# Kernel optimization log

Measured on AMD Instinct MI355X. Metric: run time of the kernel, lower is better.

Reference implementation:

```python
import jax, jax.numpy as jnp
from jax import lax
import numpy as np

VOCAB, EMBED, HID, MAXLEN, BATCH = 50000, 512, 1024, 100, 512
FORGET_BIAS = 2.0


def setup_inputs() -> dict:
    key = jax.random.key(0)
    ks = jax.random.split(key, 12)
    s = 0.02
    input_queries = jax.random.randint(ks[0], (BATCH, MAXLEN), 0, VOCAB, dtype=jnp.int32)
    input_replies = jax.random.randint(ks[1], (BATCH, MAXLEN), 0, VOCAB, dtype=jnp.int32)
    query_lengths = jnp.maximum(jax.random.randint(ks[2], (BATCH,), 0, MAXLEN, dtype=jnp.int32), 1)
    reply_lengths = jnp.maximum(jax.random.randint(ks[3], (BATCH,), 0, MAXLEN, dtype=jnp.int32), 1)
    embeddings = jax.random.normal(ks[4], (VOCAB, EMBED), dtype=jnp.float32) * s
    # shared peephole LSTM weights (reuse=True in the original): kernel over [x; h], gate order i, j, f, o
    W = jax.random.normal(ks[5], (EMBED + HID, 4 * HID), dtype=jnp.float32) * s
    b = jnp.zeros((4 * HID,), dtype=jnp.float32)
    p_i = jax.random.normal(ks[6], (HID,), dtype=jnp.float32) * s
    p_f = jax.random.normal(ks[7], (HID,), dtype=jnp.float32) * s
    p_o = jax.random.normal(ks[8], (HID,), dtype=jnp.float32) * s
    M = jax.random.normal(ks[9], (HID, HID), dtype=jnp.float32) * s
    return {
        "embeddings": embeddings, "W": W, "b": b,
        "p_i": p_i, "p_f": p_f, "p_o": p_o, "M": M,
        "input_queries": input_queries, "input_replies": input_replies,
        "query_lengths": query_lengths, "reply_lengths": reply_lengths,
    }


def _lstm_encode(x_emb, lengths, W, b, p_i, p_f, p_o):
    """Peephole LSTM (TF LSTMCell, use_peepholes=True). Returns final h at sequence_length."""
    B, L, _ = x_emb.shape
    H = p_i.shape[0]

    def step(carry, xt):
        c, h = carry
        x_t, t = xt                      # x_t: [B, E]
        z = jnp.concatenate([x_t, h], axis=-1) @ W + b   # [B, 4H]
        zi, zj, zf, zo = jnp.split(z, 4, axis=-1)
        i = jax.nn.sigmoid(zi + p_i * c)
        f = jax.nn.sigmoid(zf + FORGET_BIAS + p_f * c)
        c_new = f * c + i * jnp.tanh(zj)
        o = jax.nn.sigmoid(zo + p_o * c_new)
        h_new = o * jnp.tanh(c_new)
        valid = (t < lengths)[:, None]   # hold state past sequence_length
        return (jnp.where(valid, c_new, c), jnp.where(valid, h_new, h)), None

    init = (jnp.zeros((B, H), x_emb.dtype), jnp.zeros((B, H), x_emb.dtype))
    xs = (jnp.swapaxes(x_emb, 0, 1), jnp.arange(L, dtype=jnp.int32))
    (_, h), _ = lax.scan(step, init, xs)
    return h


def reference(embeddings, W, b, p_i, p_f, p_o, M,
              input_queries, input_replies, query_lengths, reply_lengths):
    q_emb = embeddings[input_queries]    # [B, L, E]
    r_emb = embeddings[input_replies]
    q_enc = _lstm_encode(q_emb, query_lengths, W, b, p_i, p_f, p_o)   # [B, H]
    r_enc = _lstm_encode(r_emb, reply_lengths, W, b, p_i, p_f, p_o)
    q_t = q_enc @ M                                                    # bilinear transform
    distances = q_t @ r_enc.T                                          # [B, B]
    # positives = diagonal, negatives = all off-diagonal (in-batch negatives)
    labels = jnp.eye(distances.shape[0], dtype=distances.dtype)
    # sigmoid cross entropy: softplus(x) - label * x, mean over all B*B logits
    loss = jnp.mean(jax.nn.softplus(distances) - labels * distances)
    return distances, loss
```

## Files before the change

kernel.cpp:

```cpp
#include <hip/hip_runtime.h>
#include <stdint.h>

typedef unsigned short u16;
typedef __bf16 bf16x8 __attribute__((ext_vector_type(8)));
typedef float f32x4 __attribute__((ext_vector_type(4)));

#define AS1 __attribute__((address_space(1)))
#define AS3 __attribute__((address_space(3)))

__device__ __forceinline__ void ld_lds16(const void* gp, void* lp) {
  __builtin_amdgcn_global_load_lds((AS1 void*)(void*)gp, (AS3 void*)lp, 16, 0, 0);
}

__device__ __forceinline__ u16 f2bf(float f) {
  uint32_t u = __float_as_uint(f);
  u += 0x7FFFu + ((u >> 16) & 1u);
  return (u16)(u >> 16);
}

__device__ __forceinline__ float fsig(float x) { return 1.0f / (1.0f + __expf(-x)); }
__device__ __forceinline__ float ftanhf(float x) {
  float e = __expf(-2.0f * fabsf(x));
  float t = (1.0f - e) / (1.0f + e);
  return copysignf(t, x);
}

#define LSEQ 100
#define EMB 512
#define HID 1024
#define KDIM 1536

__global__ __launch_bounds__(256, 2) void k_step(
    const u16* __restrict__ emb, const u16* __restrict__ W2T,
    const float* __restrict__ b2, const float* __restrict__ p_i,
    const float* __restrict__ p_f, const float* __restrict__ p_o,
    const int* __restrict__ tokQ, const int* __restrict__ tokR,
    const int* __restrict__ lenQ, const int* __restrict__ lenR,
    const u16* __restrict__ h_cur, u16* __restrict__ h_nxt,
    float* __restrict__ c_st, int t)
{
  __shared__ u16 sb[3 * 12288];
  const int tid = threadIdx.x;
  const int lane = tid & 63, wid = tid >> 6;
  const int wm = wid >> 1, wn = wid & 1;
  const int lane_lo = lane & 15, lane_hi = lane >> 4;
  const int g = blockIdx.x;
  const int bx = (g & 7) * 4 + ((g >> 3) & 3);
  const int by = g >> 5;

  f32x4 acc[2][4];
  const f32x4 zz = {0.f, 0.f, 0.f, 0.f};
#pragma unroll
  for (int a = 0; a < 2; ++a)
#pragma unroll
    for (int bb = 0; bb < 4; ++bb) acc[a][bb] = zz;

  int tokv[2], rowe[2], rowi[2], ldsoA[2], srcoA[2];
#pragma unroll
  for (int j = 0; j < 2; ++j) {
    const int ch = j * 256 + tid;
    const int r = ch >> 3;
    const int srcoff = ((ch & 7) ^ (r & 7)) * 8;
    const int m = by * 64 + r, e = m >> 9, i = m & 511;
    tokv[j] = (e ? tokR : tokQ)[i * LSEQ + t];
    rowe[j] = e; rowi[j] = i;
    srcoA[j] = srcoff;
    ldsoA[j] = ch * 8;
  }

  const int colbase = bx * 128 + wn * 64;
  const int h = ((colbase >> 6) << 4) + lane_lo;
  float b2v[4];
#pragma unroll
  for (int gg = 0; gg < 4; ++gg) b2v[gg] = b2[colbase + gg * 16 + lane_lo];
  const float pi = p_i[h], pf = p_f[h], po = p_o[h];
  int lenv[2][4];
  float cold[2][4];
  u16 hprev[2][4];
#pragma unroll
  for (int mi = 0; mi < 2; ++mi)
#pragma unroll
    for (int r = 0; r < 4; ++r) {
      const int m = by * 64 + wm * 32 + mi * 16 + lane_hi * 4 + r;
      const int e = m >> 9, i = m & 511;
      lenv[mi][r] = e ? lenR[i] : lenQ[i];
      const size_t ci = (size_t)(e * 512 + i) * HID + h;
      cold[mi][r] = c_st[ci];
      hprev[mi][r] = h_cur[ci];
    }
  __builtin_amdgcn_sched_barrier(0);

  const u16* pAx[2];
  const u16* pAh[2];
  const u16* pB[4];
  int ldsoB[4];
#pragma unroll
  for (int j = 0; j < 2; ++j) {
    pAx[j] = emb + (size_t)tokv[j] * EMB + srcoA[j];
    pAh[j] = h_cur + (size_t)(rowe[j] * 512 + rowi[j]) * HID - 512 + srcoA[j];
  }
#pragma unroll
  for (int j = 0; j < 4; ++j) {
    const int ch = j * 256 + tid;
    const int r = ch >> 3;
    const int srcoff = ((ch & 7) ^ (r & 7)) * 8;
    pB[j] = W2T + (size_t)(bx * 128 + r) * KDIM + srcoff;
    ldsoB[j] = ch * 8;
  }

  auto stage = [&](int kt, int buf) {
    const int kb = kt * 64;
    u16* lA = sb + buf * 12288;
    u16* lB = lA + 4096;
    const bool isx = kb < EMB;
#pragma unroll
    for (int j = 0; j < 2; ++j) ld_lds16((isx ? pAx[j] : pAh[j]) + kb, lA + ldsoA[j]);
#pragma unroll
    for (int j = 0; j < 4; ++j) ld_lds16(pB[j] + kb, lB + ldsoB[j]);
  };

  auto compute = [&](int buf) {
    const u16* lA = sb + buf * 12288;
    const u16* lB = lA + 4096;
#pragma unroll
    for (int kk = 0; kk < 2; ++kk) {
      bf16x8 aF[2], bF[4];
#pragma unroll
      for (int mi = 0; mi < 2; ++mi) {
        const int rr = wm * 32 + mi * 16 + lane_lo;
        const int byo = rr * 128 + ((kk * 64 + lane_hi * 16) ^ ((rr & 7) << 4));
        aF[mi] = *(const bf16x8*)((const char*)lA + byo);
      }
#pragma unroll
      for (int ni = 0; ni < 4; ++ni) {
        const int rr = wn * 64 + ni * 16 + lane_lo;
        const int byo = rr * 128 + ((kk * 64 + lane_hi * 16) ^ ((rr & 7) << 4));
        bF[ni] = *(const bf16x8*)((const char*)lB + byo);
      }
#pragma unroll
      for (int mi = 0; mi < 2; ++mi)
#pragma unroll
        for (int ni = 0; ni < 4; ++ni)
          acc[mi][ni] = __builtin_amdgcn_mfma_f32_16x16x32_bf16(aF[mi], bF[ni], acc[mi][ni], 0, 0, 0);
    }
  };

  stage(0, 0);
  stage(1, 1);

  for (int kt = 0; kt < 24; ++kt) {
    if (kt < 23) asm volatile("s_waitcnt vmcnt(6)" ::: "memory");
    else         asm volatile("s_waitcnt vmcnt(0)" ::: "memory");
    __builtin_amdgcn_s_barrier();
    __builtin_amdgcn_sched_barrier(0);
    if (kt < 22) stage(kt + 2, (kt + 2) % 3);
    __builtin_amdgcn_s_setprio(1);
    compute(kt % 3);
    __builtin_amdgcn_s_setprio(0);
  }

#pragma unroll
  for (int mi = 0; mi < 2; ++mi) {
#pragma unroll
    for (int r = 0; r < 4; ++r) {
      const int m = by * 64 + wm * 32 + mi * 16 + lane_hi * 4 + r;
      const int e = m >> 9, i = m & 511;
      const size_t ci = (size_t)(e * 512 + i) * HID + h;
      u16 hv;
      if (t < lenv[mi][r]) {
        const float c_old = cold[mi][r];
        const float zi = acc[mi][0][r] + b2v[0] + pi * c_old;
        const float zj = acc[mi][1][r] + b2v[1];
        const float zf = acc[mi][2][r] + b2v[2] + pf * c_old;
        const float zo = acc[mi][3][r] + b2v[3];
        const float ig = fsig(zi), fg = fsig(zf);
        const float cn = fg * c_old + ig * ftanhf(zj);
        const float og = fsig(zo + po * cn);
        const float hn = og * ftanhf(cn);
        c_st[ci] = cn;
        hv = f2bf(hn);
      } else {
        hv = hprev[mi][r];
      }
      h_nxt[ci] = hv;
    }
  }
}

template <int OUT_BF16>
__global__ __launch_bounds__(256) void k_gemm(
    const u16* __restrict__ A, const u16* __restrict__ Bn,
    void* __restrict__ Cout, int K, int ldc)
{
  __shared__ u16 lA[128 * 64];
  __shared__ u16 lB[128 * 64];
  const int tid = threadIdx.x;
  const int lane = tid & 63, wid = tid >> 6;
  const int wm = wid >> 1, wn = wid & 1;
  const int lane_lo = lane & 15, lane_hi = lane >> 4;
  const int bx = blockIdx.x, by = blockIdx.y;

  f32x4 acc[4][4];
  const f32x4 zz = {0.f, 0.f, 0.f, 0.f};
#pragma unroll
  for (int a = 0; a < 4; ++a)
#pragma unroll
    for (int bb = 0; bb < 4; ++bb) acc[a][bb] = zz;

  const int nkt = K >> 6;
  for (int kt = 0; kt < nkt; ++kt) {
    const int kb = kt * 64;
#pragma unroll
    for (int j = 0; j < 4; ++j) {
      const int cbase = (j * 4 + wid) * 64;
      const int ch = cbase + lane;
      const int r = ch >> 3;
      const int srcoff = ((((ch & 7) << 4) ^ ((r & 7) << 4)) >> 1);
      ld_lds16(A + (size_t)(by * 128 + r) * K + kb + srcoff, &lA[cbase * 8]);
    }
#pragma unroll
    for (int j = 0; j < 4; ++j) {
      const int cbase = (j * 4 + wid) * 64;
      const int ch = cbase + lane;
      const int r = ch >> 3;
      const int srcoff = ((((ch & 7) << 4) ^ ((r & 7) << 4)) >> 1);
      ld_lds16(Bn + (size_t)(bx * 128 + r) * K + kb + srcoff, &lB[cbase * 8]);
    }
    __syncthreads();
#pragma unroll
    for (int kk = 0; kk < 2; ++kk) {
      bf16x8 aF[4], bF[4];
#pragma unroll
      for (int mi = 0; mi < 4; ++mi) {
        const int rr = wm * 64 + mi * 16 + lane_lo;
        const int byo = rr * 128 + ((kk * 64 + lane_hi * 16) ^ ((rr & 7) << 4));
        aF[mi] = *(const bf16x8*)((const char*)lA + byo);
      }
#pragma unroll
      for (int ni = 0; ni < 4; ++ni) {
        const int rr = wn * 64 + ni * 16 + lane_lo;
        const int byo = rr * 128 + ((kk * 64 + lane_hi * 16) ^ ((rr & 7) << 4));
        bF[ni] = *(const bf16x8*)((const char*)lB + byo);
      }
#pragma unroll
      for (int mi = 0; mi < 4; ++mi)
#pragma unroll
        for (int ni = 0; ni < 4; ++ni)
          acc[mi][ni] = __builtin_amdgcn_mfma_f32_16x16x32_bf16(aF[mi], bF[ni], acc[mi][ni], 0, 0, 0);
    }
    __syncthreads();
  }

#pragma unroll
  for (int mi = 0; mi < 4; ++mi)
#pragma unroll
    for (int r = 0; r < 4; ++r) {
      const int m = by * 128 + wm * 64 + mi * 16 + lane_hi * 4 + r;
#pragma unroll
      for (int ni = 0; ni < 4; ++ni) {
        const int col = bx * 128 + wn * 64 + ni * 16 + lane_lo;
        const float v = acc[mi][ni][r];
        if (OUT_BF16) ((u16*)Cout)[(size_t)m * ldc + col] = f2bf(v);
        else ((float*)Cout)[(size_t)m * ldc + col] = v;
      }
    }
}

__global__ void k_transpose(const float* __restrict__ in, u16* __restrict__ out,
                            int K_, int N_, int perm)
{
  __shared__ float tile[64][65];
  const int tid = threadIdx.x;
  const int k0 = blockIdx.y * 64, n0 = blockIdx.x * 64;
  const int c = tid & 63, rq = tid >> 6;
  for (int rr = 0; rr < 64; rr += 4)
    tile[rr + rq][c] = in[(size_t)(k0 + rr + rq) * N_ + n0 + c];
  __syncthreads();
  for (int nr0 = 0; nr0 < 64; nr0 += 4) {
    const int nr = nr0 + rq;
    const int n = n0 + nr;
    int np = n;
    if (perm) {
      const int g = n >> 10, hh = n & 1023;
      np = ((hh >> 4) << 6) + (g << 4) + (hh & 15);
    }
    out[(size_t)np * K_ + k0 + c] = f2bf(tile[c][nr]);
  }
}

__global__ void k_bias(const float* __restrict__ b, float* __restrict__ b2) {
  const int n = blockIdx.x * 256 + threadIdx.x;
  if (n < 4096) {
    const int g = n >> 10, hh = n & 1023;
    const int np = ((hh >> 4) << 6) + (g << 4) + (hh & 15);
    b2[np] = b[n] + (g == 2 ? 2.0f : 0.0f);
  }
}

__global__ void k_cvt(const float4* __restrict__ in, u16* __restrict__ out, size_t n4) {
  size_t idx = (size_t)blockIdx.x * blockDim.x + threadIdx.x;
  const size_t stride = (size_t)gridDim.x * blockDim.x;
  for (; idx < n4; idx += stride) {
    const float4 v = in[idx];
    ushort4 o;
    o.x = f2bf(v.x); o.y = f2bf(v.y); o.z = f2bf(v.z); o.w = f2bf(v.w);
    *(ushort4*)(out + idx * 4) = o;
  }
}

__global__ void k_zero(uint4* __restrict__ p, size_t n) {
  size_t idx = (size_t)blockIdx.x * blockDim.x + threadIdx.x;
  const size_t stride = (size_t)gridDim.x * blockDim.x;
  const uint4 z = {0u, 0u, 0u, 0u};
  for (; idx < n; idx += stride) p[idx] = z;
}

__global__ void k_loss1(const float* __restrict__ D, float* __restrict__ part) {
  __shared__ float sd[256];
  const int tid = threadIdx.x;
  float s = 0.f;
  for (int idx = blockIdx.x * 256 + tid; idx < 512 * 512; idx += 256 * 256) {
    const float x = D[idx];
    float sp;
    if (x > 20.f) sp = x;
    else if (x < -20.f) sp = __expf(x);
    else sp = __logf(1.0f + __expf(x));
    if ((idx >> 9) == (idx & 511)) sp -= x;
    s += sp;
  }
  sd[tid] = s;
  __syncthreads();
  for (int o = 128; o > 0; o >>= 1) { if (tid < o) sd[tid] += sd[tid + o]; __syncthreads(); }
  if (tid == 0) part[blockIdx.x] = sd[0];
}

__global__ void k_loss2(const float* __restrict__ part, float* __restrict__ out) {
  __shared__ float sd[256];
  const int tid = threadIdx.x;
  sd[tid] = part[tid];
  __syncthreads();
  for (int o = 128; o > 0; o >>= 1) { if (tid < o) sd[tid] += sd[tid + o]; __syncthreads(); }
  if (tid == 0) out[0] = sd[0] * (1.0f / (512.0f * 512.0f));
}

extern "C" void kernel_launch(void* const* d_in, const int* in_sizes, int n_in,
                              void* d_out, int out_size, void* d_ws, size_t ws_size,
                              hipStream_t stream)
{
  const float* embF = (const float*)d_in[0];
  const float* W    = (const float*)d_in[1];
  const float* b    = (const float*)d_in[2];
  const float* p_i  = (const float*)d_in[3];
  const float* p_f  = (const float*)d_in[4];
  const float* p_o  = (const float*)d_in[5];
  const float* Mm   = (const float*)d_in[6];
  const int* tokQ   = (const int*)d_in[7];
  const int* tokR   = (const int*)d_in[8];
  const int* lenQ   = (const int*)d_in[9];
  const int* lenR   = (const int*)d_in[10];
  float* out = (float*)d_out;

  char* ws = (char*)d_ws;
  const size_t OFF_EMB  = 0;
  const size_t OFF_W2T  = 51200000;
  const size_t OFF_MT   = OFF_W2T + 12582912;
  const size_t OFF_B2   = OFF_MT + 2097152;
  const size_t OFF_H    = OFF_B2 + 16384;
  const size_t OFF_C    = OFF_H + 4194304;
  const size_t OFF_QT   = OFF_C + 4194304;
  const size_t OFF_PART = OFF_QT + 1048576;
  const size_t NEED = OFF_PART + 1024;
  if (ws_size < NEED) return;

  u16* embB  = (u16*)(ws + OFF_EMB);
  u16* W2T   = (u16*)(ws + OFF_W2T);
  u16* MT    = (u16*)(ws + OFF_MT);
  float* b2  = (float*)(ws + OFF_B2);
  u16* hbuf  = (u16*)(ws + OFF_H);
  float* cst = (float*)(ws + OFF_C);
  u16* qt    = (u16*)(ws + OFF_QT);
  float* part= (float*)(ws + OFF_PART);

  k_cvt<<<dim3(2048), dim3(256), 0, stream>>>((const float4*)embF, embB, (size_t)(50000 * 512 / 4));
  k_transpose<<<dim3(64, 24), dim3(256), 0, stream>>>(W, W2T, 1536, 4096, 1);
  k_transpose<<<dim3(16, 16), dim3(256), 0, stream>>>(Mm, MT, 1024, 1024, 0);
  k_bias<<<dim3(16), dim3(256), 0, stream>>>(b, b2);
  k_zero<<<dim3(256), dim3(256), 0, stream>>>((uint4*)hbuf, 131072);
  k_zero<<<dim3(256), dim3(256), 0, stream>>>((uint4*)cst, 262144);

  const size_t HBUFSTRIDE = (size_t)2 * 512 * 1024;
  for (int t = 0; t < 100; ++t) {
    u16* hc = hbuf + (size_t)(t & 1) * HBUFSTRIDE;
    u16* hn = hbuf + (size_t)((t + 1) & 1) * HBUFSTRIDE;
    k_step<<<dim3(512), dim3(256), 0, stream>>>(embB, W2T, b2, p_i, p_f, p_o,
                                                tokQ, tokR, lenQ, lenR, hc, hn, cst, t);
  }

  k_gemm<1><<<dim3(8, 4), dim3(256), 0, stream>>>(hbuf, MT, qt, 1024, 1024);
  k_gemm<0><<<dim3(4, 4), dim3(256), 0, stream>>>(qt, hbuf + (size_t)512 * 1024, out, 1024, 512);

  k_loss1<<<dim3(256), dim3(256), 0, stream>>>(out, part);
  k_loss2<<<dim3(1), dim3(256), 0, stream>>>(part, out + 262144);
}
```

Measured before the change: 2.098 ms.

## Enlarge LSTM step tile to 128x128 with split-K warp groups and LDS reduction

The per-timestep LSTM GEMM kernel now uses 512-thread blocks, each computing a 128x128 tile instead of 64x128, so there are 256 blocks instead of 512. Within a block, two warp groups split each 64-wide K slice. Their partial accumulators are combined through LDS before the gate epilogue. Staging becomes a 4-deep ring with three loads in flight, meant to improve operand reuse and cut B-operand traffic per output. The cost is more LDS (128KB per block), an extra reduction and barrier, fewer blocks on 256 CUs, and higher register pressure.

```diff
diff --git a/kernel.cpp b/kernel.cpp
--- a/kernel.cpp
+++ b/kernel.cpp
@@ -30,7 +30,7 @@
 #define HID 1024
 #define KDIM 1536
 
-__global__ __launch_bounds__(256, 2) void k_step(
+__global__ __launch_bounds__(512, 2) void k_step(
     const u16* __restrict__ emb, const u16* __restrict__ W2T,
     const float* __restrict__ b2, const float* __restrict__ p_i,
     const float* __restrict__ p_f, const float* __restrict__ p_o,
@@ -39,29 +39,30 @@
     const u16* __restrict__ h_cur, u16* __restrict__ h_nxt,
     float* __restrict__ c_st, int t)
 {
-  __shared__ u16 sb[3 * 12288];
+  __shared__ __align__(16) u16 sb[4 * 16384];
   const int tid = threadIdx.x;
   const int lane = tid & 63, wid = tid >> 6;
-  const int wm = wid >> 1, wn = wid & 1;
+  const int kw = wid >> 2;
+  const int wm = (wid >> 1) & 1, wn = wid & 1;
   const int lane_lo = lane & 15, lane_hi = lane >> 4;
   const int g = blockIdx.x;
   const int bx = (g & 7) * 4 + ((g >> 3) & 3);
   const int by = g >> 5;
 
-  f32x4 acc[2][4];
+  f32x4 acc[4][4];
   const f32x4 zz = {0.f, 0.f, 0.f, 0.f};
 #pragma unroll
-  for (int a = 0; a < 2; ++a)
+  for (int a = 0; a < 4; ++a)
 #pragma unroll
     for (int bb = 0; bb < 4; ++bb) acc[a][bb] = zz;
 
   int tokv[2], rowe[2], rowi[2], ldsoA[2], srcoA[2];
 #pragma unroll
   for (int j = 0; j < 2; ++j) {
-    const int ch = j * 256 + tid;
+    const int ch = j * 512 + tid;
     const int r = ch >> 3;
     const int srcoff = ((ch & 7) ^ (r & 7)) * 8;
-    const int m = by * 64 + r, e = m >> 9, i = m & 511;
+    const int m = by * 128 + r, e = m >> 9, i = m & 511;
     tokv[j] = (e ? tokR : tokQ)[i * LSEQ + t];
     rowe[j] = e; rowi[j] = i;
     srcoA[j] = srcoff;
@@ -70,6 +71,7 @@
 
   const int colbase = bx * 128 + wn * 64;
   const int h = ((colbase >> 6) << 4) + lane_lo;
+  const int mo = kw * 2;
   float b2v[4];
 #pragma unroll
   for (int gg = 0; gg < 4; ++gg) b2v[gg] = b2[colbase + gg * 16 + lane_lo];
@@ -78,101 +80,123 @@
   float cold[2][4];
   u16 hprev[2][4];
 #pragma unroll
-  for (int mi = 0; mi < 2; ++mi)
+  for (int m2 = 0; m2 < 2; ++m2)
 #pragma unroll
     for (int r = 0; r < 4; ++r) {
-      const int m = by * 64 + wm * 32 + mi * 16 + lane_hi * 4 + r;
+      const int m = by * 128 + wm * 64 + (mo + m2) * 16 + lane_hi * 4 + r;
       const int e = m >> 9, i = m & 511;
-      lenv[mi][r] = e ? lenR[i] : lenQ[i];
+      lenv[m2][r] = e ? lenR[i] : lenQ[i];
       const size_t ci = (size_t)(e * 512 + i) * HID + h;
-      cold[mi][r] = c_st[ci];
-      hprev[mi][r] = h_cur[ci];
+      cold[m2][r] = c_st[ci];
+      hprev[m2][r] = h_cur[ci];
     }
   __builtin_amdgcn_sched_barrier(0);
 
   const u16* pAx[2];
   const u16* pAh[2];
-  const u16* pB[4];
-  int ldsoB[4];
+  const u16* pB[2];
+  int ldsoB[2];
 #pragma unroll
   for (int j = 0; j < 2; ++j) {
     pAx[j] = emb + (size_t)tokv[j] * EMB + srcoA[j];
     pAh[j] = h_cur + (size_t)(rowe[j] * 512 + rowi[j]) * HID - 512 + srcoA[j];
   }
 #pragma unroll
-  for (int j = 0; j < 4; ++j) {
-    const int ch = j * 256 + tid;
+  for (int j = 0; j < 2; ++j) {
+    const int ch = j * 512 + tid;
     const int r = ch >> 3;
     const int srcoff = ((ch & 7) ^ (r & 7)) * 8;
     pB[j] = W2T + (size_t)(bx * 128 + r) * KDIM + srcoff;
     ldsoB[j] = ch * 8;
   }
 
-  auto stage = [&](int kt, int buf) {
+  auto stage = [&](int kt) {
     const int kb = kt * 64;
-    u16* lA = sb + buf * 12288;
-    u16* lB = lA + 4096;
+    u16* lA = sb + (kt & 3) * 16384;
+    u16* lB = lA + 8192;
     const bool isx = kb < EMB;
 #pragma unroll
     for (int j = 0; j < 2; ++j) ld_lds16((isx ? pAx[j] : pAh[j]) + kb, lA + ldsoA[j]);
 #pragma unroll
-    for (int j = 0; j < 4; ++j) ld_lds16(pB[j] + kb, lB + ldsoB[j]);
+    for (int j = 0; j < 2; ++j) ld_lds16(pB[j] + kb, lB + ldsoB[j]);
   };
 
   auto compute = [&](int buf) {
-    const u16* lA = sb + buf * 12288;
-    const u16* lB = lA + 4096;
-#pragma unroll
-    for (int kk = 0; kk < 2; ++kk) {
-      bf16x8 aF[2], bF[4];
-#pragma unroll
-      for (int mi = 0; mi < 2; ++mi) {
-        const int rr = wm * 32 + mi * 16 + lane_lo;
-        const int byo = rr * 128 + ((kk * 64 + lane_hi * 16) ^ ((rr & 7) << 4));
-        aF[mi] = *(const bf16x8*)((const char*)lA + byo);
-      }
-#pragma unroll
-      for (int ni = 0; ni < 4; ++ni) {
-        const int rr = wn * 64 + ni * 16 + lane_lo;
-        const int byo = rr * 128 + ((kk * 64 + lane_hi * 16) ^ ((rr & 7) << 4));
-        bF[ni] = *(const bf16x8*)((const char*)lB + byo);
-      }
-#pragma unroll
-      for (int mi = 0; mi < 2; ++mi)
-#pragma unroll
-        for (int ni = 0; ni < 4; ++ni)
-          acc[mi][ni] = __builtin_amdgcn_mfma_f32_16x16x32_bf16(aF[mi], bF[ni], acc[mi][ni], 0, 0, 0);
-    }
+    const u16* lA = sb + buf * 16384;
+    const u16* lB = lA + 8192;
+    bf16x8 aF[4], bF[4];
+#pragma unroll
+    for (int mi = 0; mi < 4; ++mi) {
+      const int rr = wm * 64 + mi * 16 + lane_lo;
+      const int byo = rr * 128 + ((kw * 64 + lane_hi * 16) ^ ((rr & 7) << 4));
+      aF[mi] = *(const bf16x8*)((const char*)lA + byo);
+    }
+#pragma unroll
+    for (int ni = 0; ni < 4; ++ni) {
+      const int rr = wn * 64 + ni * 16 + lane_lo;
+      const int byo = rr * 128 + ((kw * 64 + lane_hi * 16) ^ ((rr & 7) << 4));
+      bF[ni] = *(const bf16x8*)((const char*)lB + byo);
+    }
+#pragma unroll
+    for (int mi = 0; mi < 4; ++mi)
+#pragma unroll
+      for (int ni = 0; ni < 4; ++ni)
+        acc[mi][ni] = __builtin_amdgcn_mfma_f32_16x16x32_bf16(aF[mi], bF[ni], acc[mi][ni], 0, 0, 0);
   };
 
-  stage(0, 0);
-  stage(1, 1);
+  stage(0);
+  stage(1);
+  stage(2);
 
   for (int kt = 0; kt < 24; ++kt) {
-    if (kt < 23) asm volatile("s_waitcnt vmcnt(6)" ::: "memory");
-    else         asm volatile("s_waitcnt vmcnt(0)" ::: "memory");
+    if (kt < 22)       asm volatile("s_waitcnt vmcnt(8)" ::: "memory");
+    else if (kt == 22) asm volatile("s_waitcnt vmcnt(4)" ::: "memory");
+    else               asm volatile("s_waitcnt vmcnt(0)" ::: "memory");
     __builtin_amdgcn_s_barrier();
     __builtin_amdgcn_sched_barrier(0);
-    if (kt < 22) stage(kt + 2, (kt + 2) % 3);
+    if (kt < 21) stage(kt + 3);
     __builtin_amdgcn_s_setprio(1);
-    compute(kt % 3);
+    compute(kt & 3);
     __builtin_amdgcn_s_setprio(0);
   }
 
-#pragma unroll
-  for (int mi = 0; mi < 2; ++mi) {
+  float* cmbf = (float*)sb;
+  const int pair = wm * 2 + wn;
+  {
+    float* wslot = cmbf + (pair * 2 + kw) * 2048;
+    const int mw = (kw ^ 1) * 2;
+#pragma unroll
+    for (int m2 = 0; m2 < 2; ++m2)
+#pragma unroll
+      for (int ni = 0; ni < 4; ++ni)
+        *(f32x4*)(wslot + (m2 * 4 + ni) * 256 + lane * 4) = acc[mw + m2][ni];
+  }
+  __syncthreads();
+  {
+    const float* rslot = cmbf + (pair * 2 + (kw ^ 1)) * 2048;
+#pragma unroll
+    for (int m2 = 0; m2 < 2; ++m2)
+#pragma unroll
+      for (int ni = 0; ni < 4; ++ni) {
+        const f32x4 p = *(const f32x4*)(rslot + (m2 * 4 + ni) * 256 + lane * 4);
+        acc[mo + m2][ni] += p;
+      }
+  }
+
+#pragma unroll
+  for (int m2 = 0; m2 < 2; ++m2) {
 #pragma unroll
     for (int r = 0; r < 4; ++r) {
-      const int m = by * 64 + wm * 32 + mi * 16 + lane_hi * 4 + r;
+      const int m = by * 128 + wm * 64 + (mo + m2) * 16 + lane_hi * 4 + r;
       const int e = m >> 9, i = m & 511;
       const size_t ci = (size_t)(e * 512 + i) * HID + h;
       u16 hv;
-      if (t < lenv[mi][r]) {
-        const float c_old = cold[mi][r];
-        const float zi = acc[mi][0][r] + b2v[0] + pi * c_old;
-        const float zj = acc[mi][1][r] + b2v[1];
-        const float zf = acc[mi][2][r] + b2v[2] + pf * c_old;
-        const float zo = acc[mi][3][r] + b2v[3];
+      if (t < lenv[m2][r]) {
+        const float c_old = cold[m2][r];
+        const float zi = acc[mo + m2][0][r] + b2v[0] + pi * c_old;
+        const float zj = acc[mo + m2][1][r] + b2v[1];
+        const float zf = acc[mo + m2][2][r] + b2v[2] + pf * c_old;
+        const float zo = acc[mo + m2][3][r] + b2v[3];
         const float ig = fsig(zi), fg = fsig(zf);
         const float cn = fg * c_old + ig * ftanhf(zj);
         const float og = fsig(zo + po * cn);
@@ -180,7 +204,7 @@
         c_st[ci] = cn;
         hv = f2bf(hn);
       } else {
-        hv = hprev[mi][r];
+        hv = hprev[m2][r];
       }
       h_nxt[ci] = hv;
     }
@@ -392,7 +416,7 @@
   for (int t = 0; t < 100; ++t) {
     u16* hc = hbuf + (size_t)(t & 1) * HBUFSTRIDE;
     u16* hn = hbuf + (size_t)((t + 1) & 1) * HBUFSTRIDE;
-    k_step<<<dim3(512), dim3(256), 0, stream>>>(embB, W2T, b2, p_i, p_f, p_o,
+    k_step<<<dim3(256), dim3(512), 0, stream>>>(embB, W2T, b2, p_i, p_f, p_o,
                                                 tokQ, tokR, lenQ, lenR, hc, hn, cst, t);
   }
 
```

New measurement: 5.867 ms. +179.6%, slower.
